# Performance work log

Measured on AMD Instinct MI355X. Metric: run time of the kernel, lower is better.

Reference implementation:

```python
import jax, jax.numpy as jnp
import numpy as np

B, L, E, H, D, DFF = 2, 2048, 1024, 16, 64, 4096
SCALE = D ** 0.5


def rmsnorm(x):
    # NOTE: original uses mean(x*x)**0.5 with no eps and no learned scale
    rms = jnp.sqrt(jnp.mean(x * x, axis=-1, keepdims=True))
    return x / rms


def alibi_matrix():
    i = jnp.arange(L)
    dists = -jnp.abs(i[None, :] - i[:, None]).astype(jnp.float32)  # [L, L]
    slopes = 2.0 ** (-jnp.linspace(1.0, 8.0, H))                   # [H]
    alibi = slopes[:, None, None] * dists                          # [H, L, L]
    causal = jnp.tril(jnp.ones((L, L), dtype=bool))
    return jnp.where(causal[None], alibi, -jnp.inf)[None]          # [1, H, L, L]


def setup_inputs() -> dict:
    key = jax.random.key(0)
    ks = jax.random.split(key, 16)
    s = 0.02
    return {
        "X": jax.random.normal(ks[0], (B, L, E), jnp.float32),
        "encoder_out": jax.random.normal(ks[1], (B, L, E), jnp.float32),
        # self-attention params
        "Wqkv": jax.random.normal(ks[2], (E, 3 * H * D), jnp.float32) * s,
        "bqkv": jnp.zeros((3 * H * D,), jnp.float32),
        "Wo_sa": jax.random.normal(ks[3], (H * D, E), jnp.float32) * s,
        "bo_sa": jnp.zeros((E,), jnp.float32),
        # cross-attention params (computed by torch module but its forward returns X, so unused)
        "Wq": jax.random.normal(ks[4], (E, H * D), jnp.float32) * s,
        "bq": jnp.zeros((H * D,), jnp.float32),
        "Wkv": jax.random.normal(ks[5], (E, 2 * H * D), jnp.float32) * s,
        "bkv": jnp.zeros((2 * H * D,), jnp.float32),
        "Wo_ca": jax.random.normal(ks[6], (H * D, E), jnp.float32) * s,
        "bo_ca": jnp.zeros((E,), jnp.float32),
        # GLU FFN params (bias=False)
        "Ww": jax.random.normal(ks[7], (E, DFF), jnp.float32) * s,
        "Wv": jax.random.normal(ks[8], (E, DFF), jnp.float32) * s,
        "Wout": jax.random.normal(ks[9], (DFF, E), jnp.float32) * s,
    }


def reference(X, encoder_out, Wqkv, bqkv, Wo_sa, bo_sa, Wq, bq, Wkv, bkv,
              Wo_ca, bo_ca, Ww, Wv, Wout):
    alibi = alibi_matrix()

    # ---- self-attention (pre-norm + residual) ----
    h = rmsnorm(X)
    qkv = (h @ Wqkv + bqkv).reshape(B, L, H, 3, D)
    Q, K, V = qkv[..., 0, :], qkv[..., 1, :], qkv[..., 2, :]      # [B, L, H, D]
    scores = jnp.einsum('blhd,bmhd->bhlm', Q, K) / SCALE + alibi  # [B, H, L, L]
    attn = jax.nn.softmax(scores, axis=-1)
    ctx = jnp.einsum('bhlm,bmhd->blhd', attn, V).reshape(B, L, H * D)
    X = X + ctx @ Wo_sa + bo_sa

    # ---- cross-attention stage ----
    # Faithful to source: CrossAttention.forward returns its input X (the
    # normalized tensor) rather than the attention output, so this block is
    # X + rmsnorm(X). Cross-attn params never affect the output.
    X = X + rmsnorm(X)

    # ---- GLU FFN (pre-norm + residual), exact (erf) GELU as in torch F.gelu ----
    h = rmsnorm(X)
    ff = jax.nn.gelu(h @ Ww, approximate=False) * (h @ Wv)
    X = X + ff @ Wout
    return X
```

## Files before the change

### kernel.cpp

```cpp
#include <hip/hip_runtime.h>

#define B_SZ 2
#define L_SEQ 2048
#define E_DIM 1024
#define NH 16
#define DH 64
#define DFF_DIM 4096
#define ROWS (B_SZ * L_SEQ)
#define NCID 80

typedef __attribute__((ext_vector_type(8))) short short8;
typedef __attribute__((ext_vector_type(4))) float f32x4;

__device__ __forceinline__ short f2bf(float f) {
  unsigned u = __builtin_bit_cast(unsigned, f);
  u = (u + 0x7FFFu + ((u >> 16) & 1u)) >> 16;
  return (short)u;
}
__device__ __forceinline__ float bf2f(short s) {
  unsigned u = ((unsigned)(unsigned short)s) << 16;
  return __builtin_bit_cast(float, u);
}

__device__ __forceinline__ float fast_gelu(float x) {
  float ax = fabsf(x) * 0.70710678118654752f;
  float t = __builtin_amdgcn_rcpf(__builtin_fmaf(0.3275911f, ax, 1.0f));
  float p = t * __builtin_fmaf(
                    t,
                    __builtin_fmaf(
                        t,
                        __builtin_fmaf(t,
                                       __builtin_fmaf(t, 1.061405429f,
                                                      -1.453152027f),
                                       1.421413741f),
                        -0.284496736f),
                    0.254829592f);
  float erf = 1.0f - p * __expf(-ax * ax);
  erf = copysignf(erf, x);
  return 0.5f * x * (1.0f + erf);
}

__device__ __forceinline__ void async_copy16(const void* g, void* l) {
  __builtin_amdgcn_global_load_lds(
      (const __attribute__((address_space(1))) void*)g,
      (__attribute__((address_space(3))) void*)l, 16, 0, 0);
}

__device__ __forceinline__ float block_sum256(float v) {
  __shared__ float sbuf[4];
#pragma unroll
  for (int off = 32; off > 0; off >>= 1) v += __shfl_xor(v, off, 64);
  int lane = threadIdx.x & 63, w = threadIdx.x >> 6;
  if (lane == 0) sbuf[w] = v;
  __syncthreads();
  return sbuf[0] + sbuf[1] + sbuf[2] + sbuf[3];
}

__global__ __launch_bounds__(256) void prep_all(
    const float* __restrict__ Wqkv, const float* __restrict__ Wo,
    const float* __restrict__ Ww, const float* __restrict__ Wv,
    const float* __restrict__ Wout, const float* __restrict__ X,
    short* __restrict__ Bqkv3, short* __restrict__ WoT,
    short* __restrict__ Bcat, short* __restrict__ WoutT,
    short* __restrict__ H) {
  __shared__ float tile[32][33];
  int b = blockIdx.x;
  if (b < 16384) {
    const float* W;
    short* Wt;
    int K, N, mode, bx, by;
    if (b < 3072) {
      W = Wqkv; Wt = Bqkv3; K = 1024; N = 3072; mode = 1;
      bx = b % 96; by = b / 96;
    } else if (b < 4096) {
      int c = b - 3072;
      W = Wo; Wt = WoT; K = 1024; N = 1024; mode = 1;
      bx = c & 31; by = c >> 5;
    } else if (b < 8192) {
      int c = b - 4096;
      W = Ww; Wt = Bcat; K = 1024; N = 4096; mode = 2;
      bx = c & 127; by = c >> 7;
    } else if (b < 12288) {
      int c = b - 8192;
      W = Wv; Wt = Bcat; K = 1024; N = 4096; mode = 3;
      bx = c & 127; by = c >> 7;
    } else {
      int c = b - 12288;
      W = Wout; Wt = WoutT; K = 4096; N = 1024; mode = 1;
      bx = c & 31; by = c >> 5;
    }
    int n0 = bx * 32, k0 = by * 32;
    int tx = threadIdx.x & 31, ty = threadIdx.x >> 5;
#pragma unroll
    for (int i = 0; i < 4; i++)
      tile[ty + 8 * i][tx] = W[(size_t)(k0 + ty + 8 * i) * N + n0 + tx];
    __syncthreads();
#pragma unroll
    for (int i = 0; i < 4; i++) {
      int n = n0 + ty + 8 * i;
      int orow = (mode == 1)
                     ? n
                     : ((n >> 5) * 64 + (n & 31) + (mode == 3 ? 32 : 0));
      Wt[(size_t)orow * K + k0 + tx] = f2bf(tile[tx][ty + 8 * i]);
    }
  } else {
    size_t row = b - 16384;
    float4 v = ((const float4*)(X + row * E_DIM))[threadIdx.x];
    float ss = v.x * v.x + v.y * v.y + v.z * v.z + v.w * v.w;
    ss = block_sum256(ss);
    float inv = rsqrtf(ss * (1.0f / E_DIM));
    short* h = H + row * E_DIM + (size_t)threadIdx.x * 4;
    h[0] = f2bf(v.x * inv);
    h[1] = f2bf(v.y * inv);
    h[2] = f2bf(v.z * inv);
    h[3] = f2bf(v.w * inv);
  }
}

__global__ __launch_bounds__(256) void resid_rms_fused(
    const float* __restrict__ X, const float* __restrict__ P0,
    const float* __restrict__ P1, const float* __restrict__ bias,
    float* __restrict__ Xout, short* __restrict__ H) {
  size_t row = blockIdx.x;
  int t = threadIdx.x;
  float4 v = ((const float4*)(X + row * E_DIM))[t];
  float4 a = ((const float4*)(P0 + row * E_DIM))[t];
  float4 b = ((const float4*)(P1 + row * E_DIM))[t];
  float4 c = ((const float4*)bias)[t];
  v.x += a.x + b.x + c.x;
  v.y += a.y + b.y + c.y;
  v.z += a.z + b.z + c.z;
  v.w += a.w + b.w + c.w;
  float ss = v.x * v.x + v.y * v.y + v.z * v.z + v.w * v.w;
  ss = block_sum256(ss);
  float inv = rsqrtf(ss * (1.0f / E_DIM));
  float4 o;
  o.x = v.x * (1.0f + inv);
  o.y = v.y * (1.0f + inv);
  o.z = v.z * (1.0f + inv);
  o.w = v.w * (1.0f + inv);
  ((float4*)(Xout + row * E_DIM))[t] = o;
  short* h = H + row * E_DIM + (size_t)t * 4;
  h[0] = f2bf(v.x * inv);
  h[1] = f2bf(v.y * inv);
  h[2] = f2bf(v.z * inv);
  h[3] = f2bf(v.w * inv);
}

__global__ __launch_bounds__(256) void add2_k(const float* __restrict__ P0,
                                              const float* __restrict__ P1,
                                              float* __restrict__ out) {
  size_t i = (size_t)blockIdx.x * 256 + threadIdx.x;
  float4 v = ((const float4*)out)[i];
  float4 a = ((const float4*)P0)[i];
  float4 b = ((const float4*)P1)[i];
  v.x += a.x + b.x;
  v.y += a.y + b.y;
  v.z += a.z + b.z;
  v.w += a.w + b.w;
  ((float4*)out)[i] = v;
}

__global__ __launch_bounds__(256, 2) void gemm_bt(
    const short* __restrict__ A, const short* __restrict__ Bt,
    const float* __restrict__ bias, void* __restrict__ out,
    void* __restrict__ out2, void* __restrict__ out3, int M, int N, int K,
    int epi, int ksplit) {
  __shared__ short smem[128 * 32 * 4];
  short* As0 = smem;
  short* Bs0 = smem + 4096;
  short* As1 = smem + 8192;
  short* Bs1 = smem + 12288;
  int t = threadIdx.x;
  int lane = t & 63;
  int quad = lane >> 4, l16 = lane & 15;
  int wave = t >> 6;
  int wr = wave >> 1, wc = wave & 1;
  int m0 = blockIdx.y * 128, n0 = blockIdx.x * 128;
  int klen = K / ksplit;
  int kstart = blockIdx.z * klen;

  f32x4 acc[4][4];
#pragma unroll
  for (int i = 0; i < 4; i++)
#pragma unroll
    for (int j = 0; j < 4; j++) acc[i][j] = (f32x4){0.f, 0.f, 0.f, 0.f};

  for (int k0 = kstart; k0 < kstart + klen; k0 += 64) {
    __syncthreads();
#pragma unroll
    for (int p = 0; p < 2; p++) {
      int s = p * 256 + t;
      int mm = s >> 2, kk = (s & 3) * 8;
      const short* ag = A + (size_t)(m0 + mm) * K + k0 + kk;
      const short* bg = Bt + (size_t)(n0 + mm) * K + k0 + kk;
      async_copy16(ag, As0 + (size_t)s * 8);
      async_copy16(bg, Bs0 + (size_t)s * 8);
      async_copy16(ag + 32, As1 + (size_t)s * 8);
      async_copy16(bg + 32, Bs1 + (size_t)s * 8);
    }
    __syncthreads();
#pragma unroll
    for (int half = 0; half < 2; half++) {
      const short* As = half ? As1 : As0;
      const short* Bs = half ? Bs1 : Bs0;
      short8 af[4], bfv[4];
#pragma unroll
      for (int i = 0; i < 4; i++) {
        af[i] = *(const short8*)&As[(wr * 64 + i * 16 + l16) * 32 + quad * 8];
        bfv[i] = *(const short8*)&Bs[(wc * 64 + i * 16 + l16) * 32 + quad * 8];
      }
#pragma unroll
      for (int mi = 0; mi < 4; mi++)
#pragma unroll
        for (int ni = 0; ni < 4; ni++)
          acc[mi][ni] = __builtin_amdgcn_mfma_f32_16x16x32_bf16(
              af[mi], bfv[ni], acc[mi][ni], 0, 0, 0);
    }
  }

  if (epi == 5) {
    short* FF = (short*)out;
    int ffbase = blockIdx.x * 64 + wc * 32;
#pragma unroll
    for (int mi = 0; mi < 4; mi++)
#pragma unroll
      for (int ni = 0; ni < 2; ni++)
#pragma unroll
        for (int r = 0; r < 4; r++) {
          int rowl = wr * 64 + mi * 16 + quad * 4 + r;
          float g = fast_gelu(acc[mi][ni][r]);
          FF[(size_t)(m0 + rowl) * DFF_DIM + ffbase + ni * 16 + l16] =
              f2bf(g * acc[mi][ni + 2][r]);
        }
    return;
  }

#pragma unroll
  for (int mi = 0; mi < 4; mi++) {
#pragma unroll
    for (int ni = 0; ni < 4; ni++) {
      int col = n0 + wc * 64 + ni * 16 + l16;
#pragma unroll
      for (int r = 0; r < 4; r++) {
        int row = m0 + wr * 64 + mi * 16 + quad * 4 + r;
        float v = acc[mi][ni][r];
        if (epi == 4) {
          float* po = (float*)out + (size_t)blockIdx.z * ((size_t)M * N);
          po[(size_t)row * N + col] = v;
        } else {
          v += bias[col];
          int h = col / 192;
          int rem = col - h * 192;
          int ty = rem >> 6, d = rem & 63;
          short* dst = (ty == 0) ? (short*)out
                                 : ((ty == 1) ? (short*)out2 : (short*)out3);
          int bb = row >> 11, l = row & 2047;
          dst[((size_t)(bb * NH + h) * L_SEQ + l) * DH + d] = f2bf(v);
        }
      }
    }
  }
}

__global__ __launch_bounds__(512, 2) void gemm256(
    const short* __restrict__ A, const short* __restrict__ Bt,
    const float* __restrict__ bias, void* __restrict__ out,
    void* __restrict__ out2, void* __restrict__ out3, int M, int N, int K,
    int epi) {
  __shared__ __align__(16) short smem[65536];
  (void)M;
  (void)N;
  int t = threadIdx.x;
  int lane = t & 63;
  int quad = lane >> 4, l16 = lane & 15;
  int wave = t >> 6;
  int wr = wave >> 2;
  int wc = wave & 3;
  int m0 = blockIdx.y * 256, n0 = blockIdx.x * 256;

  int row0 = t >> 3;
  int sl = (t & 7) ^ (row0 & 7);
  int goff = row0 * K + sl * 8;
  int ldw = t * 16;
  char* smc = (char*)smem;
  auto stageHT = [&](const short* gsrc, int ldsbase) {
    async_copy16(gsrc + goff, smc + ldsbase + ldw);
    async_copy16(gsrc + goff + (K << 6), smc + ldsbase + 8192 + ldw);
  };

  int swz = (l16 & 7) << 4;
  int colp0 = (quad * 16) ^ swz;
  int colp1 = (64 + quad * 16) ^ swz;
  const char* aB = smc + wr * 16384 + l16 * 128;
  const char* bB = smc + 32768 + (wc >> 1) * 16384 + (wc & 1) * 8192 +
                   l16 * 128;

  f32x4 acc[8][4];
#pragma unroll
  for (int i = 0; i < 8; i++)
#pragma unroll
    for (int j = 0; j < 4; j++) acc[i][j] = (f32x4){0.f, 0.f, 0.f, 0.f};
  short8 areg[4][2], breg[4][2];

  const short* Am0 = A + (size_t)m0 * K;
  const short* Am1 = A + (size_t)(m0 + 128) * K;
  const short* Bn0 = Bt + (size_t)n0 * K;
  const short* Bn1 = Bt + (size_t)(n0 + 128) * K;

  stageHT(Am0, 0);
  stageHT(Am1, 16384);
  stageHT(Bn0, 32768);
  stageHT(Bn1, 49152);
  stageHT(Bn0 + 64, 98304);
  stageHT(Bn1 + 64, 114688);
  asm volatile("s_waitcnt vmcnt(4)" ::: "memory");
  __builtin_amdgcn_s_barrier();

  int NJ = K >> 7;
  for (int j = 0; j < NJ; ++j) {
    int kb = j << 7;
    bool lastI = (j == NJ - 1);
#pragma unroll
    for (int ph = 0; ph < 8; ++ph) {
      const int sub = ph & 3;
      const int mq = sub >> 1;
      const int nq = sub & 1;
      const int dOff = (ph >> 2) ? 65536 : 0;
      if (sub == 0 || sub == 2) {
#pragma unroll
        for (int im = 0; im < 4; ++im) {
          areg[im][0] =
              *(const short8*)(aB + dOff + (mq * 4 + im) * 2048 + colp0);
          areg[im][1] =
              *(const short8*)(aB + dOff + (mq * 4 + im) * 2048 + colp1);
        }
      }
      if (sub <= 1) {
#pragma unroll
        for (int in = 0; in < 2; ++in) {
          breg[nq * 2 + in][0] =
              *(const short8*)(bB + dOff + (nq * 2 + in) * 2048 + colp0);
          breg[nq * 2 + in][1] =
              *(const short8*)(bB + dOff + (nq * 2 + in) * 2048 + colp1);
        }
      }
      if (ph == 0) stageHT(Am0 + kb + 64, 65536);
      if (ph == 1) stageHT(Am1 + kb + 64, 65536 + 16384);
      if (!lastI) {
        if (ph == 2) stageHT(Bn0 + kb + 128, 32768);
        if (ph == 3) stageHT(Bn1 + kb + 128, 49152);
        if (ph == 4) stageHT(Am0 + kb + 128, 0);
        if (ph == 5) stageHT(Am1 + kb + 128, 16384);
        if (ph == 6) stageHT(Bn0 + kb + 192, 98304);
        if (ph == 7) stageHT(Bn1 + kb + 192, 114688);
      }
      __builtin_amdgcn_s_barrier();
      asm volatile("s_waitcnt lgkmcnt(0)" ::: "memory");
      __builtin_amdgcn_sched_barrier(0);
      __builtin_amdgcn_s_setprio(1);
#pragma unroll
      for (int im = 0; im < 4; ++im)
#pragma unroll
        for (int in = 0; in < 2; ++in)
#pragma unroll
          for (int kh = 0; kh < 2; ++kh)
            acc[mq * 4 + im][nq * 2 + in] =
                __builtin_amdgcn_mfma_f32_16x16x32_bf16(
                    areg[im][kh], breg[nq * 2 + in][kh],
                    acc[mq * 4 + im][nq * 2 + in], 0, 0, 0);
      __builtin_amdgcn_s_setprio(0);
      if (ph == 3) {
        if (lastI)
          asm volatile("s_waitcnt vmcnt(0)" ::: "memory");
        else
          asm volatile("s_waitcnt vmcnt(4)" ::: "memory");
      }
      if (ph == 7 && !lastI)
        asm volatile("s_waitcnt vmcnt(4)" ::: "memory");
      __builtin_amdgcn_s_barrier();
    }
  }

  if (epi == 5) {
    short* FF = (short*)out;
    int ffbase = (n0 + wc * 64) >> 1;
#pragma unroll
    for (int mi = 0; mi < 8; ++mi)
#pragma unroll
      for (int ni = 0; ni < 2; ++ni)
#pragma unroll
        for (int r = 0; r < 4; ++r) {
          int rowl = wr * 128 + mi * 16 + quad * 4 + r;
          float g = fast_gelu(acc[mi][ni][r]);
          FF[(size_t)(m0 + rowl) * DFF_DIM + ffbase + ni * 16 + l16] =
              f2bf(g * acc[mi][ni + 2][r]);
        }
    return;
  }
#pragma unroll
  for (int mi = 0; mi < 8; ++mi) {
#pragma unroll
    for (int ni = 0; ni < 4; ++ni) {
      int col = n0 + wc * 64 + ni * 16 + l16;
      float bv = bias[col];
      int h = col / 192;
      int rem = col - h * 192;
      int ty = rem >> 6, d = rem & 63;
      short* dst =
          (ty == 0) ? (short*)out : ((ty == 1) ? (short*)out2 : (short*)out3);
#pragma unroll
      for (int r = 0; r < 4; ++r) {
        int row = m0 + wr * 128 + mi * 16 + quad * 4 + r;
        float v = acc[mi][ni][r] + bv;
        int bb = row >> 11, l = row & 2047;
        dst[((size_t)(bb * NH + h) * L_SEQ + l) * DH + d] = f2bf(v);
      }
    }
  }
}

__global__ __launch_bounds__(256) void v_transp(const short* __restrict__ Vh,
                                                short* __restrict__ VTh) {
  int lt = blockIdx.x, bh = blockIdx.y;
  __shared__ short vtile[64 * 72];
  int t = threadIdx.x;
  int r = t >> 3, c = (t & 7) * 8;
  const short* src = Vh + ((size_t)bh * L_SEQ + lt * 64) * DH;
#pragma unroll
  for (int p = 0; p < 2; p++) {
    int row = r + p * 32;
    short8 vv = *(const short8*)(src + (size_t)row * DH + c);
    *(short8*)&vtile[row * 72 + c] = vv;
  }
  __syncthreads();
#pragma unroll
  for (int p = 0; p < 2; p++) {
    int d = r + p * 32;
    short8 o;
#pragma unroll
    for (int u = 0; u < 8; u++) o[u] = vtile[(c + u) * 72 + d];
    *(short8*)(VTh + ((size_t)bh * DH + d) * L_SEQ + lt * 64 + c) = o;
  }
}

__global__ __launch_bounds__(256) void attn_k(const short* __restrict__ Qh,
                                              const short* __restrict__ Kh,
                                              const short* __restrict__ VTh,
                                              float* __restrict__ OP,
                                              float* __restrict__ RS) {
  int cid = blockIdx.x;
  int bh = blockIdx.y;
  int b = bh >> 4, h = bh & 15;
  int qt, ch;
  if (cid < 8) {
    qt = cid; ch = 0;
  } else if (cid < 24) {
    qt = 8 + ((cid - 8) >> 1); ch = (cid - 8) & 1;
  } else if (cid < 48) {
    qt = 16 + (cid - 24) / 3; ch = (cid - 24) % 3;
  } else {
    qt = 24 + ((cid - 48) >> 2); ch = (cid - 48) & 3;
  }
  int t0 = ch * 8;
  int tend = min(t0 + 8, qt + 1);

  int t = threadIdx.x;
  int wave = t >> 6, lane = t & 63;
  int quad = lane >> 4, l16 = lane & 15;

  __shared__ short kt[128 * 72];
  __shared__ short vt[64 * 136];
  __shared__ short pb[4 * 16 * 70];

  const float L2E = 1.4426950408889634f;
  const float slope = exp2f(-(1.0f + (7.0f / 15.0f) * (float)h));
  const float slopeL = slope * L2E;
  int iw = qt * 64 + wave * 16;

  short8 qf[2];
  {
    const short* qp = Qh + ((size_t)bh * L_SEQ + iw + l16) * DH + quad * 8;
    qf[0] = *(const short8*)(qp);
    qf[1] = *(const short8*)(qp + 32);
  }

  f32x4 o[4];
#pragma unroll
  for (int i = 0; i < 4; i++) o[i] = (f32x4){0.f, 0.f, 0.f, 0.f};
  float rs[4] = {0.f, 0.f, 0.f, 0.f};
  float crow[4];
  int irow[4];
#pragma unroll
  for (int r = 0; r < 4; r++) {
    irow[r] = iw + quad * 4 + r;
    crow[r] = -slopeL * (float)irow[r] - 8.0f * L2E;
  }

  int sr = t >> 3, sc = (t & 7) * 8;
  const short* kg = Kh + (size_t)bh * L_SEQ * DH;
  const short* vg = VTh + (size_t)bh * DH * L_SEQ;
  short8 kreg[4], vreg[4];
  auto loadKV = [&](int j0) {
    kreg[0] = *(const short8*)(kg + (size_t)(j0 + sr) * DH + sc);
    kreg[1] = *(const short8*)(kg + (size_t)(j0 + sr + 32) * DH + sc);
    kreg[2] = *(const short8*)(kg + (size_t)(j0 + sr + 64) * DH + sc);
    kreg[3] = *(const short8*)(kg + (size_t)(j0 + sr + 96) * DH + sc);
    vreg[0] = *(const short8*)(vg + (size_t)sr * L_SEQ + j0 + sc);
    vreg[1] = *(const short8*)(vg + (size_t)(sr + 32) * L_SEQ + j0 + sc);
    vreg[2] = *(const short8*)(vg + (size_t)sr * L_SEQ + j0 + 64 + sc);
    vreg[3] = *(const short8*)(vg + (size_t)(sr + 32) * L_SEQ + j0 + 64 + sc);
  };
  loadKV(t0 * 64);

  short* pw = &pb[wave * 16 * 70];
  for (int tp = t0; tp < tend; tp += 2) {
    __syncthreads();
    *(short8*)&kt[sr * 72 + sc] = kreg[0];
    *(short8*)&kt[(sr + 32) * 72 + sc] = kreg[1];
    *(short8*)&kt[(sr + 64) * 72 + sc] = kreg[2];
    *(short8*)&kt[(sr + 96) * 72 + sc] = kreg[3];
    *(short8*)&vt[sr * 136 + sc] = vreg[0];
    *(short8*)&vt[(sr + 32) * 136 + sc] = vreg[1];
    *(short8*)&vt[sr * 136 + 64 + sc] = vreg[2];
    *(short8*)&vt[(sr + 32) * 136 + 64 + sc] = vreg[3];
    __syncthreads();
    if (tp + 2 < tend) loadKV((tp + 2) * 64);
    int te = min(tp + 2, tend);
    for (int tix = tp; tix < te; ++tix) {
      int sub = tix - tp;
      int j0 = tix * 64;
      f32x4 s[4];
      __builtin_amdgcn_s_setprio(1);
#pragma unroll
      for (int nt = 0; nt < 4; nt++) {
        f32x4 a = (f32x4){0.f, 0.f, 0.f, 0.f};
#pragma unroll
        for (int ks = 0; ks < 2; ks++) {
          short8 bf = *(const short8*)&kt[(sub * 64 + nt * 16 + l16) * 72 +
                                          ks * 32 + quad * 8];
          a = __builtin_amdgcn_mfma_f32_16x16x32_bf16(qf[ks], bf, a, 0, 0, 0);
        }
        s[nt] = a;
      }
      __builtin_amdgcn_s_setprio(0);
      bool diag = (tix == qt);
#pragma unroll
      for (int nt = 0; nt < 4; nt++) {
        int j = j0 + nt * 16 + l16;
        float jb = slopeL * (float)j;
#pragma unroll
        for (int r = 0; r < 4; r++) {
          float v = __builtin_fmaf(s[nt][r], 0.18033688011117129f,
                                   jb + crow[r]);
          if (diag && j > irow[r]) v = -1e30f;
          float p = exp2f(v);
          rs[r] += p;
          pw[(quad * 4 + r) * 70 + nt * 16 + l16] = f2bf(p);
        }
      }
      short8 pf[2];
      pf[0] = *(const short8*)&pw[l16 * 70 + quad * 8];
      pf[1] = *(const short8*)&pw[l16 * 70 + 32 + quad * 8];
      __builtin_amdgcn_s_setprio(1);
#pragma unroll
      for (int nt = 0; nt < 4; nt++) {
#pragma unroll
        for (int ks = 0; ks < 2; ks++) {
          short8 bv = *(const short8*)&vt[(nt * 16 + l16) * 136 + sub * 64 +
                                          ks * 32 + quad * 8];
          o[nt] = __builtin_amdgcn_mfma_f32_16x16x32_bf16(pf[ks], bv, o[nt],
                                                          0, 0, 0);
        }
      }
      __builtin_amdgcn_s_setprio(0);
    }
  }
  float* op = OP + ((size_t)bh * NCID + cid) * 64 * 64;
  float* rsp = RS + ((size_t)bh * NCID + cid) * 64;
#pragma unroll
  for (int r = 0; r < 4; r++) {
#pragma unroll
    for (int off = 1; off < 16; off <<= 1) rs[r] += __shfl_xor(rs[r], off, 64);
    int rowl = wave * 16 + quad * 4 + r;
#pragma unroll
    for (int nt = 0; nt < 4; nt++) op[rowl * 64 + nt * 16 + l16] = o[nt][r];
    if (l16 == 0) rsp[rowl] = rs[r];
  }
}

__global__ __launch_bounds__(256) void attn_merge(const float* __restrict__ OP,
                                                  const float* __restrict__ RS,
                                                  short* __restrict__ ctx) {
  int row = blockIdx.x;
  int b = row >> 11, i = row & 2047;
  int qt = i >> 6, rowin = i & 63;
  int base, nch;
  if (qt < 8) {
    base = qt; nch = 1;
  } else if (qt < 16) {
    base = 8 + 2 * (qt - 8); nch = 2;
  } else if (qt < 24) {
    base = 24 + 3 * (qt - 16); nch = 3;
  } else {
    base = 48 + 4 * (qt - 24); nch = 4;
  }
  int t = threadIdx.x;
  int col = t * 4;
  int h = col >> 6;
  int bh = b * NH + h;
  float4 o = {0.f, 0.f, 0.f, 0.f};
  float l = 0.f;
  for (int s = 0; s < nch; s++) {
    size_t cb = ((size_t)bh * NCID + base + s) * 64 + rowin;
    float4 v = *(const float4*)&OP[cb * 64 + (col & 63)];
    o.x += v.x;
    o.y += v.y;
    o.z += v.z;
    o.w += v.w;
    l += RS[cb];
  }
  float inv = 1.0f / l;
  short* dst = ctx + (size_t)row * (NH * DH) + col;
  dst[0] = f2bf(o.x * inv);
  dst[1] = f2bf(o.y * inv);
  dst[2] = f2bf(o.z * inv);
  dst[3] = f2bf(o.w * inv);
}

extern "C" void kernel_launch(void* const* d_in, const int* in_sizes, int n_in,
                              void* d_out, int out_size, void* d_ws,
                              size_t ws_size, hipStream_t stream) {
  const float* X = (const float*)d_in[0];
  const float* Wqkv = (const float*)d_in[2];
  const float* bqkv = (const float*)d_in[3];
  const float* Wo_sa = (const float*)d_in[4];
  const float* bo_sa = (const float*)d_in[5];
  const float* Ww = (const float*)d_in[12];
  const float* Wv = (const float*)d_in[13];
  const float* Wout = (const float*)d_in[14];

  char* ws = (char*)d_ws;
  auto take = [&](size_t bytes) {
    char* p = ws;
    ws += (bytes + 255) & ~(size_t)255;
    return p;
  };
  short* Bqkv3 = (short*)take((size_t)3072 * 1024 * 2);
  short* WoT = (short*)take((size_t)E_DIM * E_DIM * 2);
  short* Bcat = (short*)take((size_t)2 * DFF_DIM * E_DIM * 2);
  short* WoutT = (short*)take((size_t)E_DIM * DFF_DIM * 2);
  short* Hbuf = (short*)take((size_t)ROWS * E_DIM * 2);
  short* Qh = (short*)take((size_t)ROWS * NH * DH * 2);
  short* Kh = (short*)take((size_t)ROWS * NH * DH * 2);
  short* Vh = (short*)take((size_t)ROWS * NH * DH * 2);
  short* VTh = (short*)take((size_t)ROWS * NH * DH * 2);
  short* CTX = (short*)take((size_t)ROWS * NH * DH * 2);
  char* big = take((size_t)48 * 1024 * 1024);
  float* OP = (float*)big;
  float* RS = OP + (size_t)B_SZ * NH * NCID * 64 * 64;
  float* Pwo = (float*)(big + (size_t)16 * 1024 * 1024);
  short* FF = (short*)Pwo;
  float* Pwout = (float*)Qh;
  (void)ws_size;
  (void)in_sizes;
  (void)n_in;
  (void)out_size;

  dim3 blk(256);
  prep_all<<<16384 + ROWS, blk, 0, stream>>>(Wqkv, Wo_sa, Ww, Wv, Wout, X,
                                             Bqkv3, WoT, Bcat, WoutT, Hbuf);
  gemm256<<<dim3(3072 / 256, ROWS / 256), dim3(512), 0, stream>>>(
      Hbuf, Bqkv3, bqkv, Qh, Kh, Vh, ROWS, 3072, 1024, 6);
  v_transp<<<dim3(L_SEQ / 64, B_SZ * NH), blk, 0, stream>>>(Vh, VTh);
  attn_k<<<dim3(NCID, B_SZ * NH), blk, 0, stream>>>(Qh, Kh, VTh, OP, RS);
  attn_merge<<<ROWS, blk, 0, stream>>>(OP, RS, CTX);
  gemm_bt<<<dim3(1024 / 128, ROWS / 128, 2), blk, 0, stream>>>(
      CTX, WoT, nullptr, Pwo, nullptr, nullptr, ROWS, 1024, 1024, 4, 2);
  resid_rms_fused<<<ROWS, blk, 0, stream>>>(
      X, Pwo, Pwo + (size_t)ROWS * E_DIM, bo_sa, (float*)d_out, Hbuf);
  gemm256<<<dim3(2 * DFF_DIM / 256, ROWS / 256), dim3(512), 0, stream>>>(
      Hbuf, Bcat, nullptr, FF, nullptr, nullptr, ROWS, 2 * DFF_DIM, 1024, 5);
  gemm_bt<<<dim3(1024 / 128, ROWS / 128, 2), blk, 0, stream>>>(
      FF, WoutT, nullptr, Pwout, nullptr, nullptr, ROWS, 1024, 4096, 4, 2);
  add2_k<<<ROWS * E_DIM / (256 * 4), blk, 0, stream>>>(
      Pwout, Pwout + (size_t)ROWS * E_DIM, (float*)d_out);
}
```

Before: 425.0 us.

## Compute transposed S tile and pass P to PV MFMA via shuffles, not LDS

The QK^T MFMA now takes its operands in swapped order, so each lane holds scores for one query row across four consecutive keys. The softmax probabilities are packed to bf16 pairs in registers and redistributed with cross-lane shuffles into the PV MFMA A-operand layout. This replaces the per-wave LDS scratch write and read-back of P, and the row-sum reduction drops from four 4-step shuffle trees to two shuffles. In exchange it adds 16 shuffles plus selects per key tile and depends on the shuffle index mapping being exactly right for correctness.

Measured after the change: 408.2 us. 1.04x faster.

```diff
diff --git a/kernel.cpp b/kernel.cpp
--- a/kernel.cpp
+++ b/kernel.cpp
@@ -20,6 +20,10 @@
 __device__ __forceinline__ float bf2f(short s) {
   unsigned u = ((unsigned)(unsigned short)s) << 16;
   return __builtin_bit_cast(float, u);
+}
+__device__ __forceinline__ unsigned pack2bf(float lo, float hi) {
+  return ((unsigned)(unsigned short)f2bf(hi) << 16) |
+         (unsigned)(unsigned short)f2bf(lo);
 }
 
 __device__ __forceinline__ float fast_gelu(float x) {
@@ -451,7 +455,7 @@
                                               float* __restrict__ RS) {
   int cid = blockIdx.x;
   int bh = blockIdx.y;
-  int b = bh >> 4, h = bh & 15;
+  int h = bh & 15;
   int qt, ch;
   if (cid < 8) {
     qt = cid; ch = 0;
@@ -471,7 +475,6 @@
 
   __shared__ short kt[128 * 72];
   __shared__ short vt[64 * 136];
-  __shared__ short pb[4 * 16 * 70];
 
   const float L2E = 1.4426950408889634f;
   const float slope = exp2f(-(1.0f + (7.0f / 15.0f) * (float)h));
@@ -488,14 +491,9 @@
   f32x4 o[4];
 #pragma unroll
   for (int i = 0; i < 4; i++) o[i] = (f32x4){0.f, 0.f, 0.f, 0.f};
-  float rs[4] = {0.f, 0.f, 0.f, 0.f};
-  float crow[4];
-  int irow[4];
-#pragma unroll
-  for (int r = 0; r < 4; r++) {
-    irow[r] = iw + quad * 4 + r;
-    crow[r] = -slopeL * (float)irow[r] - 8.0f * L2E;
-  }
+  float rs = 0.f;
+  const int irow = iw + l16;
+  const float base_l = -slopeL * (float)irow - 8.0f * L2E;
 
   int sr = t >> 3, sc = (t & 7) * 8;
   const short* kg = Kh + (size_t)bh * L_SEQ * DH;
@@ -513,7 +511,9 @@
   };
   loadKV(t0 * 64);
 
-  short* pw = &pb[wave * 16 * 70];
+  const int sA = l16 + ((quad & 1) << 5);
+  const int sB = sA + 16;
+
   for (int tp = t0; tp < tend; tp += 2) {
     __syncthreads();
     *(short8*)&kt[sr * 72 + sc] = kreg[0];
@@ -537,56 +537,89 @@
         f32x4 a = (f32x4){0.f, 0.f, 0.f, 0.f};
 #pragma unroll
         for (int ks = 0; ks < 2; ks++) {
-          short8 bf = *(const short8*)&kt[(sub * 64 + nt * 16 + l16) * 72 +
+          short8 kf = *(const short8*)&kt[(sub * 64 + nt * 16 + l16) * 72 +
                                           ks * 32 + quad * 8];
-          a = __builtin_amdgcn_mfma_f32_16x16x32_bf16(qf[ks], bf, a, 0, 0, 0);
+          a = __builtin_amdgcn_mfma_f32_16x16x32_bf16(kf, qf[ks], a, 0, 0, 0);
         }
         s[nt] = a;
       }
       __builtin_amdgcn_s_setprio(0);
       bool diag = (tix == qt);
+      unsigned w[4][2];
 #pragma unroll
       for (int nt = 0; nt < 4; nt++) {
-        int j = j0 + nt * 16 + l16;
-        float jb = slopeL * (float)j;
+        int jb_i = j0 + nt * 16 + quad * 4;
+        float jb = __builtin_fmaf(slopeL, (float)jb_i, base_l);
+        float pv[4];
 #pragma unroll
         for (int r = 0; r < 4; r++) {
           float v = __builtin_fmaf(s[nt][r], 0.18033688011117129f,
-                                   jb + crow[r]);
-          if (diag && j > irow[r]) v = -1e30f;
+                                   jb + slopeL * (float)r);
+          if (diag && jb_i + r > irow) v = -1e30f;
           float p = exp2f(v);
-          rs[r] += p;
-          pw[(quad * 4 + r) * 70 + nt * 16 + l16] = f2bf(p);
+          rs += p;
+          pv[r] = p;
         }
-      }
-      short8 pf[2];
-      pf[0] = *(const short8*)&pw[l16 * 70 + quad * 8];
-      pf[1] = *(const short8*)&pw[l16 * 70 + 32 + quad * 8];
+        w[nt][0] = pack2bf(pv[0], pv[1]);
+        w[nt][1] = pack2bf(pv[2], pv[3]);
+      }
+      bool hiq = (quad & 2) != 0;
+      union {
+        unsigned u[4];
+        short8 v;
+      } pk0, pk1;
+      {
+        unsigned x0 = __shfl((int)w[0][0], sA, 64);
+        unsigned y0 = __shfl((int)w[1][0], sA, 64);
+        pk0.u[0] = hiq ? y0 : x0;
+        unsigned x1 = __shfl((int)w[0][1], sA, 64);
+        unsigned y1 = __shfl((int)w[1][1], sA, 64);
+        pk0.u[1] = hiq ? y1 : x1;
+        unsigned x2 = __shfl((int)w[0][0], sB, 64);
+        unsigned y2 = __shfl((int)w[1][0], sB, 64);
+        pk0.u[2] = hiq ? y2 : x2;
+        unsigned x3 = __shfl((int)w[0][1], sB, 64);
+        unsigned y3 = __shfl((int)w[1][1], sB, 64);
+        pk0.u[3] = hiq ? y3 : x3;
+        unsigned z0 = __shfl((int)w[2][0], sA, 64);
+        unsigned q0 = __shfl((int)w[3][0], sA, 64);
+        pk1.u[0] = hiq ? q0 : z0;
+        unsigned z1 = __shfl((int)w[2][1], sA, 64);
+        unsigned q1 = __shfl((int)w[3][1], sA, 64);
+        pk1.u[1] = hiq ? q1 : z1;
+        unsigned z2 = __shfl((int)w[2][0], sB, 64);
+        unsigned q2 = __shfl((int)w[3][0], sB, 64);
+        pk1.u[2] = hiq ? q2 : z2;
+        unsigned z3 = __shfl((int)w[2][1], sB, 64);
+        unsigned q3 = __shfl((int)w[3][1], sB, 64);
+        pk1.u[3] = hiq ? q3 : z3;
+      }
       __builtin_amdgcn_s_setprio(1);
 #pragma unroll
       for (int nt = 0; nt < 4; nt++) {
-#pragma unroll
-        for (int ks = 0; ks < 2; ks++) {
-          short8 bv = *(const short8*)&vt[(nt * 16 + l16) * 136 + sub * 64 +
-                                          ks * 32 + quad * 8];
-          o[nt] = __builtin_amdgcn_mfma_f32_16x16x32_bf16(pf[ks], bv, o[nt],
-                                                          0, 0, 0);
-        }
+        short8 bv0 = *(const short8*)&vt[(nt * 16 + l16) * 136 + sub * 64 +
+                                         quad * 8];
+        o[nt] = __builtin_amdgcn_mfma_f32_16x16x32_bf16(pk0.v, bv0, o[nt], 0,
+                                                        0, 0);
+        short8 bv1 = *(const short8*)&vt[(nt * 16 + l16) * 136 + sub * 64 +
+                                         32 + quad * 8];
+        o[nt] = __builtin_amdgcn_mfma_f32_16x16x32_bf16(pk1.v, bv1, o[nt], 0,
+                                                        0, 0);
       }
       __builtin_amdgcn_s_setprio(0);
     }
   }
+  rs += __shfl_xor(rs, 16, 64);
+  rs += __shfl_xor(rs, 32, 64);
   float* op = OP + ((size_t)bh * NCID + cid) * 64 * 64;
   float* rsp = RS + ((size_t)bh * NCID + cid) * 64;
 #pragma unroll
   for (int r = 0; r < 4; r++) {
-#pragma unroll
-    for (int off = 1; off < 16; off <<= 1) rs[r] += __shfl_xor(rs[r], off, 64);
     int rowl = wave * 16 + quad * 4 + r;
 #pragma unroll
     for (int nt = 0; nt < 4; nt++) op[rowl * 64 + nt * 16 + l16] = o[nt][r];
-    if (l16 == 0) rsp[rowl] = rs[r];
-  }
+  }
+  if (quad == 0) rsp[wave * 16 + l16] = rs;
 }
 
 __global__ __launch_bounds__(256) void attn_merge(const float* __restrict__ OP,
```
